# Performance work log

Measured on AMD Instinct MI355X. Metric: run time of the kernel, lower is better.

The kernel has to match this reference:

```python
import jax, jax.numpy as jnp
import numpy as np

D_IN, D_H, D_OUT = 1024, 1024, 1024
D_MOE = 4096
N_EXPERTS = 8
TOP_K = 2


def setup_inputs() -> dict:
    key = jax.random.key(0)
    ks = jax.random.split(key, 10)
    s = lambda d: 1.0 / np.sqrt(d)
    x = jax.random.normal(ks[0], (2, 2048, D_IN), dtype=jnp.float32)
    W_in = jax.random.normal(ks[1], (D_IN, D_H), dtype=jnp.float32) * s(D_IN)
    b_in = jnp.zeros((D_H,), jnp.float32)
    W_gate = jax.random.normal(ks[2], (D_H, N_EXPERTS), dtype=jnp.float32) * s(D_H)
    b_gate = jnp.zeros((N_EXPERTS,), jnp.float32)
    W1 = jax.random.normal(ks[3], (N_EXPERTS, D_H, D_MOE), dtype=jnp.float32) * s(D_H)
    b1 = jnp.zeros((N_EXPERTS, D_MOE), jnp.float32)
    W2 = jax.random.normal(ks[4], (N_EXPERTS, D_MOE, D_H), dtype=jnp.float32) * s(D_MOE)
    b2 = jnp.zeros((N_EXPERTS, D_H), jnp.float32)
    W_out = jax.random.normal(ks[5], (D_H, D_OUT), dtype=jnp.float32) * s(D_H)
    b_out = jnp.zeros((D_OUT,), jnp.float32)
    return {"x": x, "W_in": W_in, "b_in": b_in, "W_gate": W_gate, "b_gate": b_gate,
            "W1": W1, "b1": b1, "W2": W2, "b2": b2, "W_out": W_out, "b_out": b_out}


def reference(x, W_in, b_in, W_gate, b_gate, W1, b1, W2, b2, W_out, b_out):
    B, S, _ = x.shape
    h = x @ W_in + b_in                       # [B,S,D_H]
    t = h.reshape(B * S, -1)                  # tokens [N,D_H]

    # --- top-k softmax gating ---
    logits = t @ W_gate + b_gate              # [N,E]
    probs = jax.nn.softmax(logits, axis=-1)
    topv, topi = jax.lax.top_k(probs, TOP_K)  # [N,k]
    topv = topv / jnp.sum(topv, axis=-1, keepdims=True)
    # dense routing weights [N,E] (zeros for unselected experts)
    route = jnp.zeros_like(probs).at[jnp.arange(t.shape[0])[:, None], topi].set(topv)

    # --- expert MLPs (dense all-expert compute, weighted combine) ---
    mid = jax.nn.relu(jnp.einsum('nd,edh->neh', t, W1) + b1)   # [N,E,D_MOE]
    eout = jnp.einsum('neh,ehd->ned', mid, W2) + b2            # [N,E,D_H]
    moe_out = jnp.einsum('ne,ned->nd', route, eout)            # [N,D_H]

    out = moe_out.reshape(B, S, -1) @ W_out + b_out            # [B,S,D_OUT]
    return out
```

## Files before the change

### kernel.cpp

```cpp
#include <hip/hip_runtime.h>
#include <hip/hip_bf16.h>

typedef __bf16 bf16_t;
typedef bf16_t bf16x8 __attribute__((ext_vector_type(8)));
typedef bf16_t bf16x4 __attribute__((ext_vector_type(4)));
typedef float f32x4 __attribute__((ext_vector_type(4)));

#define DIN 1024
#define DH 1024
#define DMOE 4096
#define NEXP 8
#define NTOK 4096

__device__ __forceinline__ void gload_lds16(const bf16_t* g, bf16_t* l) {
  __builtin_amdgcn_global_load_lds(
      (const __attribute__((address_space(1))) void*)g,
      (__attribute__((address_space(3))) void*)l, 16, 0, 0);
}


__global__ void k_zero8(int* p) {
  if (threadIdx.x < 8) p[threadIdx.x] = 0;
}

__global__ void k_transpose_cvt(const float* __restrict__ src, bf16_t* __restrict__ dst,
                                int R, int C) {
  __shared__ float tile[64][65];
  const size_t mofs = (size_t)blockIdx.z * R * C;
  const float* s = src + mofs;
  bf16_t* d = dst + mofs;
  const int c0 = blockIdx.x * 64, r0 = blockIdx.y * 64;
  const int t = threadIdx.x;
  const int rr = t >> 4;
  const int cc = (t & 15) << 2;
#pragma unroll
  for (int i = 0; i < 64; i += 16) {
    const float4 v = *(const float4*)&s[(size_t)(r0 + rr + i) * C + c0 + cc];
    tile[rr + i][cc + 0] = v.x;
    tile[rr + i][cc + 1] = v.y;
    tile[rr + i][cc + 2] = v.z;
    tile[rr + i][cc + 3] = v.w;
  }
  __syncthreads();
  const int oc = t >> 4;
  const int orr = (t & 15) << 2;
#pragma unroll
  for (int i = 0; i < 64; i += 16) {
    bf16x4 o;
    o.x = (bf16_t)tile[orr + 0][oc + i];
    o.y = (bf16_t)tile[orr + 1][oc + i];
    o.z = (bf16_t)tile[orr + 2][oc + i];
    o.w = (bf16_t)tile[orr + 3][oc + i];
    *(bf16x4*)&d[(size_t)(c0 + oc + i) * R + r0 + orr] = o;
  }
}

__global__ void k_cvt_bf16(const float* __restrict__ src, bf16_t* __restrict__ dst, int n4) {
  const int i = blockIdx.x * blockDim.x + threadIdx.x;
  if (i < n4) {
    const float4 v = *(const float4*)(src + (size_t)i * 4);
    bf16x4 o;
    o.x = (bf16_t)v.x; o.y = (bf16_t)v.y; o.z = (bf16_t)v.z; o.w = (bf16_t)v.w;
    *(bf16x4*)(dst + (size_t)i * 4) = o;
  }
}

__global__ void k_gate_prep(const float* __restrict__ Win, const float* __restrict__ Wgate,
                            const float* __restrict__ b_in, const float* __restrict__ b_gate,
                            double* __restrict__ G, double* __restrict__ cvec) {
  const int lane = threadIdx.x & 63;
  const int wave = (blockIdx.x * blockDim.x + threadIdx.x) >> 6;
  const int nw = (gridDim.x * blockDim.x) >> 6;
  for (int d = wave; d <= DIN; d += nw) {
    const float* row = (d < DIN) ? (Win + (size_t)d * DH) : b_in;
    double acc[8] = {0, 0, 0, 0, 0, 0, 0, 0};
    for (int k = lane; k < DH; k += 64) {
      const double xv = (double)row[k];
      const float* g = Wgate + (size_t)k * NEXP;
#pragma unroll
      for (int ee = 0; ee < 8; ++ee) acc[ee] += xv * (double)g[ee];
    }
#pragma unroll
    for (int ee = 0; ee < 8; ++ee) {
      double a = acc[ee];
      for (int o = 32; o > 0; o >>= 1) a += __shfl_down(a, o);
      acc[ee] = a;
    }
    if (lane == 0) {
      if (d < DIN) {
#pragma unroll
        for (int ee = 0; ee < 8; ++ee) G[(size_t)d * 8 + ee] = acc[ee];
      } else {
#pragma unroll
        for (int ee = 0; ee < 8; ++ee) cvec[ee] = acc[ee] + (double)b_gate[ee];
      }
    }
  }
}

__global__ void k_gating(const float* __restrict__ x, const double* __restrict__ G,
                         const double* __restrict__ cvec, int* __restrict__ cnt,
                         int* __restrict__ list, float* __restrict__ wlist) {
  const int lane = threadIdx.x & 63;
  const int t = blockIdx.x * (blockDim.x >> 6) + (threadIdx.x >> 6);
  if (t >= NTOK) return;
  const float* xr = x + (size_t)t * DIN;
  double acc[8] = {0, 0, 0, 0, 0, 0, 0, 0};
  for (int d = lane; d < DIN; d += 64) {
    const double xv = (double)xr[d];
    const double* g = G + (size_t)d * 8;
#pragma unroll
    for (int ee = 0; ee < 8; ++ee) acc[ee] += xv * g[ee];
  }
#pragma unroll
  for (int ee = 0; ee < 8; ++ee) {
    double a = acc[ee];
    for (int o = 32; o > 0; o >>= 1) a += __shfl_down(a, o);
    acc[ee] = a;
  }
  if (lane == 0) {
    double l[8];
#pragma unroll
    for (int ee = 0; ee < 8; ++ee) l[ee] = acc[ee] + cvec[ee];
    double m = l[0];
#pragma unroll
    for (int ee = 1; ee < 8; ++ee) m = fmax(m, l[ee]);
    double p[8];
#pragma unroll
    for (int ee = 0; ee < 8; ++ee) p[ee] = exp(l[ee] - m);
    int i1 = 0;
#pragma unroll
    for (int ee = 1; ee < 8; ++ee)
      if (p[ee] > p[i1]) i1 = ee;
    int i2 = (i1 == 0) ? 1 : 0;
#pragma unroll
    for (int ee = 0; ee < 8; ++ee)
      if (ee != i1 && p[ee] > p[i2]) i2 = ee;
    const double s2 = p[i1] + p[i2];
    const float w1 = (float)(p[i1] / s2);
    const float w2 = (float)(p[i2] / s2);
    int lp = atomicAdd(&cnt[i1], 1);
    list[i1 * NTOK + lp] = t * 2;
    wlist[i1 * NTOK + lp] = w1;
    lp = atomicAdd(&cnt[i2], 1);
    list[i2 * NTOK + lp] = t * 2 + 1;
    wlist[i2 * NTOK + lp] = w2;
  }
}

__global__ void k_scan(const int* __restrict__ cnt, int* __restrict__ offs) {
  if (threadIdx.x == 0) {
    int s = 0;
    for (int e = 0; e < NEXP; ++e) { offs[e] = s; s += cnt[e]; }
    offs[NEXP] = s;
  }
}

__global__ void k_combine(const float* __restrict__ eout, bf16_t* __restrict__ moebf) {
  const int i = blockIdx.x * blockDim.x + threadIdx.x;
  const int t = i >> 8;
  const int q = (i & 255) * 4;
  const float4 a = *(const float4*)(eout + ((size_t)t * 2) * DH + q);
  const float4 b = *(const float4*)(eout + ((size_t)t * 2 + 1) * DH + q);
  bf16x4 o;
  o.x = (bf16_t)(a.x + b.x); o.y = (bf16_t)(a.y + b.y);
  o.z = (bf16_t)(a.z + b.z); o.w = (bf16_t)(a.w + b.w);
  *(bf16x4*)(moebf + (size_t)t * DH + q) = o;
}

template <int MODE>
__global__ __launch_bounds__(256, 3) void k_gemm(
    const bf16_t* __restrict__ Abase, const bf16_t* __restrict__ Bbase,
    const float* __restrict__ biasBase, void* __restrict__ Cbase,
    int M, int N, int K,
    const int* __restrict__ cnt, const int* __restrict__ offs,
    const int* __restrict__ listBase, const float* __restrict__ wlistBase) {
  const int e = blockIdx.z;
  const int mblk = blockIdx.y, nblk = blockIdx.x;
  int Mloc = M;
  const bf16_t* A = Abase;
  const bf16_t* B = Bbase;
  const float* bias = biasBase;
  const int* myList = nullptr;
  const float* myW = nullptr;
  int rowOff = 0;
  if constexpr (MODE == 1 || MODE == 2) {
    Mloc = cnt[e];
    if (mblk * 128 >= Mloc) return;
    B = Bbase + (size_t)e * N * K;
    bias = biasBase + (size_t)e * N;
    myList = listBase + e * NTOK;
    myW = wlistBase + e * NTOK;
    rowOff = offs[e];
    if constexpr (MODE == 2) A = Abase + (size_t)rowOff * K;
  }

  __shared__ bf16_t As[3][128 * 32];
  __shared__ bf16_t Bs[3][128 * 32];

  const int tid = threadIdx.x;
  const int lane = tid & 63;
  const int wid = tid >> 6;
  const int wr = wid >> 1, wc = wid & 1;

  const int srow0 = wid * 32 + (lane >> 2);
  const int srow1 = srow0 + 16;
  const int skcol = ((lane & 3) ^ ((lane >> 3) & 3)) * 8;

  int ar0 = mblk * 128 + srow0;
  int ar1 = mblk * 128 + srow1;
  if constexpr (MODE == 1 || MODE == 2) {
    if (ar0 > Mloc - 1) ar0 = Mloc - 1;
    if (ar1 > Mloc - 1) ar1 = Mloc - 1;
  }
  size_t arow0 = (size_t)ar0, arow1 = (size_t)ar1;
  if constexpr (MODE == 1) {
    arow0 = (size_t)(myList[ar0] >> 1);
    arow1 = (size_t)(myList[ar1] >> 1);
  }
  const bf16_t* aptr0 = A + arow0 * K + skcol;
  const bf16_t* aptr1 = A + arow1 * K + skcol;
  const bf16_t* bptr0 = B + (size_t)(nblk * 128 + srow0) * K + skcol;
  const bf16_t* bptr1 = B + (size_t)(nblk * 128 + srow1) * K + skcol;

  const int ldsOfsA0 = (wid * 32) * 32;
  const int ldsOfsA1 = (wid * 32 + 16) * 32;

  f32x4 acc[4][4] = {};

  const int nkt = K >> 5;

  auto stage = [&](int buf, int kt) {
    const size_t ko = (size_t)kt * 32;
    gload_lds16(aptr0 + ko, &As[buf][ldsOfsA0]);
    gload_lds16(aptr1 + ko, &As[buf][ldsOfsA1]);
    gload_lds16(bptr0 + ko, &Bs[buf][ldsOfsA0]);
    gload_lds16(bptr1 + ko, &Bs[buf][ldsOfsA1]);
  };

  stage(0, 0);
  if (nkt > 1) stage(1, 1);

  const int fr = lane & 15;
  const int s0 = (((lane >> 4) ^ ((fr >> 1) & 3)) << 3);

  int cur = 0;
  for (int kt = 0; kt < nkt; ++kt) {
    int nxt = cur + 2;
    if (nxt >= 3) nxt -= 3;
    if (kt + 2 < nkt) {
      stage(nxt, kt + 2);
      asm volatile("s_waitcnt vmcnt(8)" ::: "memory");
    } else if (kt + 1 < nkt) {
      asm volatile("s_waitcnt vmcnt(4)" ::: "memory");
    } else {
      asm volatile("s_waitcnt vmcnt(0)" ::: "memory");
    }
    __builtin_amdgcn_s_barrier();

    bf16x8 af[4], bfr[4];
#pragma unroll
    for (int m = 0; m < 4; ++m)
      af[m] = *(const bf16x8*)&As[cur][(wr * 64 + m * 16 + fr) * 32 + s0];
#pragma unroll
    for (int n = 0; n < 4; ++n)
      bfr[n] = *(const bf16x8*)&Bs[cur][(wc * 64 + n * 16 + fr) * 32 + s0];
#pragma unroll
    for (int m = 0; m < 4; ++m)
#pragma unroll
      for (int n = 0; n < 4; ++n)
        acc[m][n] = __builtin_amdgcn_mfma_f32_16x16x32_bf16(af[m], bfr[n], acc[m][n], 0, 0, 0);

    __builtin_amdgcn_s_barrier();
    cur += 1;
    if (cur >= 3) cur -= 3;
  }

  const int colBase = nblk * 128 + wc * 64 + (lane & 15);
  const int rowBase = mblk * 128 + wr * 64 + ((lane >> 4) << 2);
#pragma unroll
  for (int n = 0; n < 4; ++n) {
    const int c = colBase + n * 16;
    const float bv = bias[c];
#pragma unroll
    for (int m = 0; m < 4; ++m) {
#pragma unroll
      for (int j = 0; j < 4; ++j) {
        const int r = rowBase + m * 16 + j;
        float v = acc[m][n][j] + bv;
        if constexpr (MODE == 0) {
          ((bf16_t*)Cbase)[(size_t)r * N + c] = (bf16_t)v;
        } else if constexpr (MODE == 1) {
          if (r < Mloc) {
            v = fmaxf(v, 0.0f);
            ((bf16_t*)Cbase)[(size_t)(rowOff + r) * N + c] = (bf16_t)v;
          }
        } else if constexpr (MODE == 2) {
          if (r < Mloc) {
            const int entry = myList[r];
            const float w = myW[r];
            ((float*)Cbase)[(size_t)entry * DH + c] = v * w;
          }
        } else {
          ((float*)Cbase)[(size_t)r * N + c] = v;
        }
      }
    }
  }
}


extern "C" void kernel_launch(void* const* d_in, const int* in_sizes, int n_in,
                              void* d_out, int out_size, void* d_ws, size_t ws_size,
                              hipStream_t stream) {
  const float* x      = (const float*)d_in[0];
  const float* W_in   = (const float*)d_in[1];
  const float* b_in   = (const float*)d_in[2];
  const float* W_gate = (const float*)d_in[3];
  const float* b_gate = (const float*)d_in[4];
  const float* W1     = (const float*)d_in[5];
  const float* b1     = (const float*)d_in[6];
  const float* W2     = (const float*)d_in[7];
  const float* b2     = (const float*)d_in[8];
  const float* W_out  = (const float*)d_in[9];
  const float* b_out  = (const float*)d_in[10];

  char* ws = (char*)d_ws;
  size_t off = 0;
  auto alloc = [&](size_t bytes) -> void* {
    void* p = ws + off;
    off += (bytes + 255) & ~(size_t)255;
    return p;
  };

  bf16_t* WtIn  = (bf16_t*)alloc((size_t)DH * DIN * 2);
  bf16_t* Wt1   = (bf16_t*)alloc((size_t)NEXP * DMOE * DH * 2);
  bf16_t* Wt2   = (bf16_t*)alloc((size_t)NEXP * DH * DMOE * 2);
  bf16_t* WtOut = (bf16_t*)alloc((size_t)DH * DH * 2);
  bf16_t* xbf   = (bf16_t*)alloc((size_t)NTOK * DIN * 2);
  bf16_t* hbf   = (bf16_t*)alloc((size_t)NTOK * DH * 2);
  bf16_t* mid   = (bf16_t*)alloc((size_t)2 * NTOK * DMOE * 2);
  float*  eout  = (float*)alloc((size_t)2 * NTOK * DH * 4);
  bf16_t* moebf = (bf16_t*)alloc((size_t)NTOK * DH * 2);
  double* G     = (double*)alloc((size_t)DIN * 8 * 8);
  double* cvec  = (double*)alloc(8 * 8);
  int*    cnt   = (int*)alloc(NEXP * 4);
  int*    offs  = (int*)alloc((NEXP + 1) * 4);
  int*    list  = (int*)alloc((size_t)NEXP * NTOK * 4);
  float*  wlist = (float*)alloc((size_t)NEXP * NTOK * 4);

  k_zero8<<<1, 64, 0, stream>>>(cnt);

  k_transpose_cvt<<<dim3(DH / 64, DIN / 64, 1), 256, 0, stream>>>(W_in, WtIn, DIN, DH);
  k_transpose_cvt<<<dim3(DMOE / 64, DH / 64, NEXP), 256, 0, stream>>>(W1, Wt1, DH, DMOE);
  k_transpose_cvt<<<dim3(DH / 64, DMOE / 64, NEXP), 256, 0, stream>>>(W2, Wt2, DMOE, DH);
  k_transpose_cvt<<<dim3(DH / 64, DH / 64, 1), 256, 0, stream>>>(W_out, WtOut, DH, DH);
  k_cvt_bf16<<<(NTOK * DIN / 4 + 255) / 256, 256, 0, stream>>>(x, xbf, NTOK * DIN / 4);

  k_gate_prep<<<64, 256, 0, stream>>>(W_in, W_gate, b_in, b_gate, G, cvec);
  k_gating<<<NTOK / 4, 256, 0, stream>>>(x, G, cvec, cnt, list, wlist);
  k_scan<<<1, 64, 0, stream>>>(cnt, offs);

  k_gemm<0><<<dim3(DH / 128, NTOK / 128, 1), 256, 0, stream>>>(
      xbf, WtIn, b_in, hbf, NTOK, DH, DIN, nullptr, nullptr, nullptr, nullptr);
  k_gemm<1><<<dim3(DMOE / 128, NTOK / 128, NEXP), 256, 0, stream>>>(
      hbf, Wt1, b1, mid, NTOK, DMOE, DH, cnt, offs, list, wlist);
  k_gemm<2><<<dim3(DH / 128, NTOK / 128, NEXP), 256, 0, stream>>>(
      mid, Wt2, b2, eout, NTOK, DH, DMOE, cnt, offs, list, wlist);
  k_combine<<<NTOK * DH / 4 / 256, 256, 0, stream>>>(eout, moebf);
  k_gemm<3><<<dim3(DH / 128, NTOK / 128, 1), 256, 0, stream>>>(
      moebf, WtOut, b_out, (float*)d_out, NTOK, DH, DH, nullptr, nullptr, nullptr, nullptr);
}
```

Measured before the change: 573.5 us.

## Scatter h into expert-packed layout so expert GEMM reads contiguous rows

Result: slower. 587.0 us (+2.3%).

```diff
diff --git a/kernel.cpp b/kernel.cpp
--- a/kernel.cpp
+++ b/kernel.cpp
@@ -154,6 +154,16 @@
     for (int e = 0; e < NEXP; ++e) { offs[e] = s; s += cnt[e]; }
     offs[NEXP] = s;
   }
+}
+
+__global__ void k_invert(const int* __restrict__ cnt, const int* __restrict__ offs,
+                         const int* __restrict__ list, int* __restrict__ packpos) {
+  const int e = blockIdx.x;
+  const int n = cnt[e];
+  const int base = offs[e];
+  const int* myList = list + e * NTOK;
+  for (int i = threadIdx.x; i < n; i += blockDim.x)
+    packpos[myList[i]] = base + i;
 }
 
 __global__ void k_combine(const float* __restrict__ eout, bf16_t* __restrict__ moebf) {
@@ -192,7 +202,7 @@
     myList = listBase + e * NTOK;
     myW = wlistBase + e * NTOK;
     rowOff = offs[e];
-    if constexpr (MODE == 2) A = Abase + (size_t)rowOff * K;
+    A = Abase + (size_t)rowOff * K;
   }
 
   __shared__ bf16_t As[3][128 * 32];
@@ -213,13 +223,8 @@
     if (ar0 > Mloc - 1) ar0 = Mloc - 1;
     if (ar1 > Mloc - 1) ar1 = Mloc - 1;
   }
-  size_t arow0 = (size_t)ar0, arow1 = (size_t)ar1;
-  if constexpr (MODE == 1) {
-    arow0 = (size_t)(myList[ar0] >> 1);
-    arow1 = (size_t)(myList[ar1] >> 1);
-  }
-  const bf16_t* aptr0 = A + arow0 * K + skcol;
-  const bf16_t* aptr1 = A + arow1 * K + skcol;
+  const bf16_t* aptr0 = A + (size_t)ar0 * K + skcol;
+  const bf16_t* aptr1 = A + (size_t)ar1 * K + skcol;
   const bf16_t* bptr0 = B + (size_t)(nblk * 128 + srow0) * K + skcol;
   const bf16_t* bptr1 = B + (size_t)(nblk * 128 + srow1) * K + skcol;
 
@@ -289,7 +294,11 @@
         const int r = rowBase + m * 16 + j;
         float v = acc[m][n][j] + bv;
         if constexpr (MODE == 0) {
-          ((bf16_t*)Cbase)[(size_t)r * N + c] = (bf16_t)v;
+          const bf16_t hv = (bf16_t)v;
+          const int p0 = listBase[2 * r];
+          const int p1 = listBase[2 * r + 1];
+          ((bf16_t*)Cbase)[(size_t)p0 * N + c] = hv;
+          ((bf16_t*)Cbase)[(size_t)p1 * N + c] = hv;
         } else if constexpr (MODE == 1) {
           if (r < Mloc) {
             v = fmaxf(v, 0.0f);
@@ -333,21 +342,22 @@
     return p;
   };
 
-  bf16_t* WtIn  = (bf16_t*)alloc((size_t)DH * DIN * 2);
-  bf16_t* Wt1   = (bf16_t*)alloc((size_t)NEXP * DMOE * DH * 2);
-  bf16_t* Wt2   = (bf16_t*)alloc((size_t)NEXP * DH * DMOE * 2);
-  bf16_t* WtOut = (bf16_t*)alloc((size_t)DH * DH * 2);
-  bf16_t* xbf   = (bf16_t*)alloc((size_t)NTOK * DIN * 2);
-  bf16_t* hbf   = (bf16_t*)alloc((size_t)NTOK * DH * 2);
-  bf16_t* mid   = (bf16_t*)alloc((size_t)2 * NTOK * DMOE * 2);
-  float*  eout  = (float*)alloc((size_t)2 * NTOK * DH * 4);
-  bf16_t* moebf = (bf16_t*)alloc((size_t)NTOK * DH * 2);
-  double* G     = (double*)alloc((size_t)DIN * 8 * 8);
-  double* cvec  = (double*)alloc(8 * 8);
-  int*    cnt   = (int*)alloc(NEXP * 4);
-  int*    offs  = (int*)alloc((NEXP + 1) * 4);
-  int*    list  = (int*)alloc((size_t)NEXP * NTOK * 4);
-  float*  wlist = (float*)alloc((size_t)NEXP * NTOK * 4);
+  bf16_t* WtIn   = (bf16_t*)alloc((size_t)DH * DIN * 2);
+  bf16_t* Wt1    = (bf16_t*)alloc((size_t)NEXP * DMOE * DH * 2);
+  bf16_t* Wt2    = (bf16_t*)alloc((size_t)NEXP * DH * DMOE * 2);
+  bf16_t* WtOut  = (bf16_t*)alloc((size_t)DH * DH * 2);
+  bf16_t* xbf    = (bf16_t*)alloc((size_t)NTOK * DIN * 2);
+  bf16_t* hpack  = (bf16_t*)alloc((size_t)2 * NTOK * DH * 2);
+  bf16_t* mid    = (bf16_t*)alloc((size_t)2 * NTOK * DMOE * 2);
+  float*  eout   = (float*)alloc((size_t)2 * NTOK * DH * 4);
+  bf16_t* moebf  = (bf16_t*)alloc((size_t)NTOK * DH * 2);
+  double* G      = (double*)alloc((size_t)DIN * 8 * 8);
+  double* cvec   = (double*)alloc(8 * 8);
+  int*    cnt    = (int*)alloc(NEXP * 4);
+  int*    offs   = (int*)alloc((NEXP + 1) * 4);
+  int*    list   = (int*)alloc((size_t)NEXP * NTOK * 4);
+  float*  wlist  = (float*)alloc((size_t)NEXP * NTOK * 4);
+  int*    packpos= (int*)alloc((size_t)2 * NTOK * 4);
 
   k_zero8<<<1, 64, 0, stream>>>(cnt);
 
@@ -360,11 +370,12 @@
   k_gate_prep<<<64, 256, 0, stream>>>(W_in, W_gate, b_in, b_gate, G, cvec);
   k_gating<<<NTOK / 4, 256, 0, stream>>>(x, G, cvec, cnt, list, wlist);
   k_scan<<<1, 64, 0, stream>>>(cnt, offs);
+  k_invert<<<NEXP, 256, 0, stream>>>(cnt, offs, list, packpos);
 
   k_gemm<0><<<dim3(DH / 128, NTOK / 128, 1), 256, 0, stream>>>(
-      xbf, WtIn, b_in, hbf, NTOK, DH, DIN, nullptr, nullptr, nullptr, nullptr);
+      xbf, WtIn, b_in, hpack, NTOK, DH, DIN, nullptr, nullptr, packpos, nullptr);
   k_gemm<1><<<dim3(DMOE / 128, NTOK / 128, NEXP), 256, 0, stream>>>(
-      hbf, Wt1, b1, mid, NTOK, DMOE, DH, cnt, offs, list, wlist);
+      hpack, Wt1, b1, mid, NTOK, DMOE, DH, cnt, offs, list, wlist);
   k_gemm<2><<<dim3(DH / 128, NTOK / 128, NEXP), 256, 0, stream>>>(
       mid, Wt2, b2, eout, NTOK, DH, DMOE, cnt, offs, list, wlist);
   k_combine<<<NTOK * DH / 4 / 256, 256, 0, stream>>>(eout, moebf);
```
